# Kernel optimization log

Hardware: AMD Instinct MI355X
Metric: run time of the kernel (lower is better)

Reference implementation:

```python
import jax, jax.numpy as jnp
import numpy as np

N = 84          # nodes; N*(N-1)/2 == 3486, hardcoded by LayerNorm shapes
P = 3486        # number of pairwise rows
H = 2048        # h_size
EPS = 1e-5


def _gru_cell(x, h, Wih, Whh, bih, bhh):
    # PyTorch GRUCell math. Wih: [3H, in], Whh: [3H, H]
    gi = x @ Wih.T + bih
    gh = h @ Whh.T + bhh
    ir, iz, inew = jnp.split(gi, 3, axis=1)
    hr, hz, hnew = jnp.split(gh, 3, axis=1)
    r = jax.nn.sigmoid(ir + hr)
    z = jax.nn.sigmoid(iz + hz)
    n = jnp.tanh(inew + r * hnew)
    return (1.0 - z) * n + z * h


def _full_ln(x, w, b):
    # nn.LayerNorm([3486, h]) normalizes over BOTH dims jointly (biased var)
    mu = jnp.mean(x)
    var = jnp.mean((x - mu) ** 2)
    return (x - mu) * jax.lax.rsqrt(var + EPS) * w + b


def setup_inputs() -> dict:
    key = jax.random.key(0)
    ks = jax.random.split(key, 22)
    f32 = jnp.float32

    def nrm(k, shape, std):
        return jax.random.normal(k, shape, dtype=f32) * std

    h2 = H // 2
    return {
        "x": nrm(ks[0], (N, 64), 1.0),
        "hid": nrm(ks[1], (P, H), 1.0),
        # GRUCell(64, H) parameters
        "gru_Wih": nrm(ks[2], (3 * H, 64), 1.0 / np.sqrt(64)),
        "gru_Whh": nrm(ks[3], (3 * H, H), 1.0 / np.sqrt(H)),
        "gru_bih": nrm(ks[4], (3 * H,), 0.01),
        "gru_bhh": nrm(ks[5], (3 * H,), 0.01),
        # Linear/LayerNorm stack
        "W1": nrm(ks[6], (H, H), np.sqrt(2.0 / H)),
        "b1": jnp.zeros((H,), f32),
        "ln1_w": jnp.ones((P, H), f32),
        "ln1_b": jnp.zeros((P, H), f32),
        "W2": nrm(ks[7], (h2, H), np.sqrt(2.0 / H)),
        "b2": jnp.zeros((h2,), f32),
        "ln2_w": jnp.ones((P, h2), f32),
        "ln2_b": jnp.zeros((P, h2), f32),
        "W3": nrm(ks[8], (h2, h2), np.sqrt(2.0 / h2)),
        "b3": jnp.zeros((h2,), f32),
        "ln3_w": jnp.ones((P, h2), f32),
        "ln3_b": jnp.zeros((P, h2), f32),
        "W4": nrm(ks[9], (1, h2), np.sqrt(2.0 / h2)),
        "b4": jnp.zeros((1,), f32),
    }


def reference(x, hid, gru_Wih, gru_Whh, gru_bih, gru_bhh,
              W1, b1, ln1_w, ln1_b, W2, b2, ln2_w, ln2_b,
              W3, b3, ln3_w, ln3_b, W4, b4):
    # Pairwise gather: rows ordered (0,1),(0,2),...,(0,N-1),(1,2),... -- matches
    # the torch loop of expand+cat.
    iu, ju = jnp.triu_indices(N, k=1)
    x1 = x[iu]  # [P, 64]
    x2 = x[ju]  # [P, 64]

    h = _gru_cell(x1, hid, gru_Wih, gru_Whh, gru_bih, gru_bhh)
    h = _gru_cell(x2, h, gru_Wih, gru_Whh, gru_bih, gru_bhh)

    h = _full_ln(jax.nn.relu(h @ W1.T + b1), ln1_w, ln1_b)
    h = _full_ln(jax.nn.relu(h @ W2.T + b2), ln2_w, ln2_b)
    h = _full_ln(jax.nn.relu(h @ W3.T + b3), ln3_w, ln3_b)
    vals = jax.nn.sigmoid(h @ W4.T + b4)[:, 0]  # [P]

    # Strict-upper-triangular scatter + symmetrize (equals the torch pad loop)
    M = jnp.zeros((N, N), dtype=vals.dtype).at[iu, ju].set(vals)
    return M + M.T
```

## Files before the change

kernel.cpp:

```cpp
#include <hip/hip_runtime.h>
#include <stdint.h>

#define P_PAIRS 3486
#define NNODES 84
#define HSZ 2048
#define H2SZ 1024
#define G3H 6144
#define LN_EPS 1e-5f

typedef short bf16x8 __attribute__((ext_vector_type(8)));
typedef float f32x4 __attribute__((ext_vector_type(4)));

typedef __attribute__((address_space(3))) unsigned int lds_uint;
typedef __attribute__((address_space(1))) const unsigned int global_cuint;

__device__ __forceinline__ unsigned short f2bf(float f) {
    unsigned int u = __float_as_uint(f);
    return (unsigned short)((u + 0x7fffu + ((u >> 16) & 1u)) >> 16);
}
__device__ __forceinline__ float bf2f(unsigned short s) {
    return __uint_as_float(((unsigned int)s) << 16);
}
__device__ __forceinline__ float sigm(float x) {
    return 1.f / (1.f + expf(-x));
}

#define S_WHH (G3H * HSZ / 4)
#define S_W1  (HSZ * HSZ / 4)
#define S_W2  (H2SZ * HSZ / 4)
#define S_W3  (H2SZ * H2SZ / 4)
#define S_HID (P_PAIRS * HSZ / 4)
#define B0 (S_WHH)
#define B1 (B0 + S_W1)
#define B2 (B1 + S_W2)
#define B3 (B2 + S_W3)
#define B4 (B3 + S_HID)

__device__ __forceinline__ void cvt4(const float4* in, ushort4* out, int i) {
    float4 v = in[i];
    ushort4 o;
    o.x = f2bf(v.x); o.y = f2bf(v.y); o.z = f2bf(v.z); o.w = f2bf(v.w);
    out[i] = o;
}

__global__ void k_prep(const float4* __restrict__ Whh, ushort4* __restrict__ whh_b,
                       const float4* __restrict__ W1, ushort4* __restrict__ w1_b,
                       const float4* __restrict__ W2, ushort4* __restrict__ w2_b,
                       const float4* __restrict__ W3, ushort4* __restrict__ w3_b,
                       const float4* __restrict__ hid, ushort4* __restrict__ hid_b,
                       int* __restrict__ ip, int* __restrict__ jp, float* __restrict__ acc,
                       const float* __restrict__ x, const float* __restrict__ Wih,
                       const float* __restrict__ bih, float* __restrict__ gi) {
    const int tid0 = blockIdx.x * blockDim.x + threadIdx.x;
    const int stride = gridDim.x * blockDim.x;
    int idx = tid0;
    if (idx < 8) acc[idx] = 0.f;
    if (idx < P_PAIRS) {
        int i = 0, rem = idx;
        while (rem >= NNODES - 1 - i) { rem -= NNODES - 1 - i; ++i; }
        ip[idx] = i;
        jp[idx] = i + 1 + rem;
    }
    for (; idx < B4; idx += stride) {
        if (idx < B0)      cvt4(Whh, whh_b, idx);
        else if (idx < B1) cvt4(W1, w1_b, idx - B0);
        else if (idx < B2) cvt4(W2, w2_b, idx - B1);
        else if (idx < B3) cvt4(W3, w3_b, idx - B2);
        else               cvt4(hid, hid_b, idx - B3);
    }
    for (int g = tid0; g < NNODES * G3H; g += stride) {
        int node = g / G3H, n = g - node * G3H;
        const float* xr = x + node * 64;
        const float* wr = Wih + (size_t)n * 64;
        float s = bih[n];
#pragma unroll
        for (int k = 0; k < 64; ++k) s += xr[k] * wr[k];
        gi[g] = s;
    }
}

__global__ __launch_bounds__(256)
void k_gemm(const unsigned short* __restrict__ A, const unsigned short* __restrict__ B,
            const float* __restrict__ bias, float* __restrict__ Cf,
            unsigned short* __restrict__ Cb,
            int M, int N, int K, int relu, float* __restrict__ accg, int redslot) {
    __shared__ __align__(16) unsigned short lsA[128 * 32];
    __shared__ __align__(16) unsigned short lsB[128 * 32];
    const int m0 = blockIdx.x * 128;
    const int n0 = blockIdx.y * 128;
    const int tid = threadIdx.x;
    const int lane = tid & 63;
    const int wave = tid >> 6;
    const int wr = (wave >> 1) * 64;
    const int wc = (wave & 1) * 64;
    const int fr = lane & 15;
    const int quad = lane >> 4;
    const int kof = quad * 8;

    f32x4 acc[4][4];
#pragma unroll
    for (int i = 0; i < 4; ++i)
#pragma unroll
        for (int j = 0; j < 4; ++j) {
            f32x4 z = {0.f, 0.f, 0.f, 0.f};
            acc[i][j] = z;
        }

    const int lin0 = (wave * 2) * 1024 + lane * 16;
    const int lin1 = lin0 + 1024;
    const int row0 = lin0 >> 6, col0 = (lin0 & 63) >> 1;
    const int row1 = lin1 >> 6, col1 = (lin1 & 63) >> 1;
    int ga0 = m0 + row0; if (ga0 >= M) ga0 = M - 1;
    int ga1 = m0 + row1; if (ga1 >= M) ga1 = M - 1;
    const int gb0 = n0 + row0, gb1 = n0 + row1;

    const unsigned short* pa0 = A + (size_t)ga0 * K + col0;
    const unsigned short* pa1 = A + (size_t)ga1 * K + col1;
    const unsigned short* pb0 = B + (size_t)gb0 * K + col0;
    const unsigned short* pb1 = B + (size_t)gb1 * K + col1;
    lds_uint* la0 = (lds_uint*)&lsA[(wave * 2) * 512];
    lds_uint* la1 = (lds_uint*)&lsA[(wave * 2 + 1) * 512];
    lds_uint* lb0 = (lds_uint*)&lsB[(wave * 2) * 512];
    lds_uint* lb1 = (lds_uint*)&lsB[(wave * 2 + 1) * 512];

    for (int k0 = 0; k0 < K; k0 += 32) {
        __syncthreads();
        __builtin_amdgcn_global_load_lds((global_cuint*)(pa0 + k0), la0, 16, 0, 0);
        __builtin_amdgcn_global_load_lds((global_cuint*)(pa1 + k0), la1, 16, 0, 0);
        __builtin_amdgcn_global_load_lds((global_cuint*)(pb0 + k0), lb0, 16, 0, 0);
        __builtin_amdgcn_global_load_lds((global_cuint*)(pb1 + k0), lb1, 16, 0, 0);
        __syncthreads();
        bf16x8 av[4], bv[4];
#pragma unroll
        for (int mi = 0; mi < 4; ++mi)
            av[mi] = *(const bf16x8*)(&lsA[(wr + mi * 16 + fr) * 32 + kof]);
#pragma unroll
        for (int ni = 0; ni < 4; ++ni)
            bv[ni] = *(const bf16x8*)(&lsB[(wc + ni * 16 + fr) * 32 + kof]);
#pragma unroll
        for (int mi = 0; mi < 4; ++mi)
#pragma unroll
            for (int ni = 0; ni < 4; ++ni)
                acc[mi][ni] = __builtin_amdgcn_mfma_f32_16x16x32_bf16(av[mi], bv[ni], acc[mi][ni], 0, 0, 0);
    }

    float s1 = 0.f, s2 = 0.f;
#pragma unroll
    for (int mi = 0; mi < 4; ++mi) {
#pragma unroll
        for (int r = 0; r < 4; ++r) {
            int row = m0 + wr + mi * 16 + quad * 4 + r;
            if (row >= M) continue;
#pragma unroll
            for (int ni = 0; ni < 4; ++ni) {
                int col = n0 + wc + ni * 16 + fr;
                float v = acc[mi][ni][r];
                if (bias) v += bias[col];
                if (relu) v = fmaxf(v, 0.f);
                if (redslot >= 0) { s1 += v; s2 += v * v; }
                if (Cb) Cb[(size_t)row * N + col] = f2bf(v);
                else    Cf[(size_t)row * N + col] = v;
            }
        }
    }

    if (redslot >= 0) {
        __syncthreads();
        float* sm = (float*)lsA;
        sm[tid] = s1;
        sm[256 + tid] = s2;
        __syncthreads();
        for (int o = 128; o > 0; o >>= 1) {
            if (tid < o) {
                sm[tid] += sm[tid + o];
                sm[256 + tid] += sm[256 + tid + o];
            }
            __syncthreads();
        }
        if (tid == 0) {
            atomicAdd(&accg[redslot * 2], sm[0]);
            atomicAdd(&accg[redslot * 2 + 1], sm[256]);
        }
    }
}

__global__ void k_combine(const float4* __restrict__ gi, const ushort4* __restrict__ gh,
                          const int* __restrict__ pair, const float4* __restrict__ hprev_f,
                          const ushort4* __restrict__ hprev_b,
                          ushort4* __restrict__ hout) {
    int idx = blockIdx.x * blockDim.x + threadIdx.x;
    if (idx >= P_PAIRS * (HSZ / 4)) return;
    int p = idx >> 9;
    int c4 = idx & 511;
    int node = pair[p];
    const float4* gip = gi + (size_t)node * (G3H / 4) + c4;
    const ushort4* ghp = gh + (size_t)p * (G3H / 4) + c4;
    float4 gir = gip[0],   giz = gip[512], gin = gip[1024];
    ushort4 ghr4 = ghp[0], ghz4 = ghp[512], ghn4 = ghp[1024];
    float hr[4] = {bf2f(ghr4.x), bf2f(ghr4.y), bf2f(ghr4.z), bf2f(ghr4.w)};
    float hz[4] = {bf2f(ghz4.x), bf2f(ghz4.y), bf2f(ghz4.z), bf2f(ghz4.w)};
    float hn[4] = {bf2f(ghn4.x), bf2f(ghn4.y), bf2f(ghn4.z), bf2f(ghn4.w)};
    float hp[4];
    if (hprev_f) {
        float4 h = hprev_f[idx];
        hp[0] = h.x; hp[1] = h.y; hp[2] = h.z; hp[3] = h.w;
    } else {
        ushort4 h = hprev_b[idx];
        hp[0] = bf2f(h.x); hp[1] = bf2f(h.y); hp[2] = bf2f(h.z); hp[3] = bf2f(h.w);
    }
    float ir[4] = {gir.x, gir.y, gir.z, gir.w};
    float iz[4] = {giz.x, giz.y, giz.z, giz.w};
    float in_[4] = {gin.x, gin.y, gin.z, gin.w};
    unsigned short o[4];
#pragma unroll
    for (int q = 0; q < 4; ++q) {
        float r = sigm(ir[q] + hr[q]);
        float z = sigm(iz[q] + hz[q]);
        float nn = tanhf(in_[q] + r * hn[q]);
        o[q] = f2bf((1.f - z) * nn + z * hp[q]);
    }
    ushort4 ov = {o[0], o[1], o[2], o[3]};
    hout[idx] = ov;
}

__global__ void k_lnapply(const float4* __restrict__ t, const float4* __restrict__ w,
                          const float4* __restrict__ b, const float* __restrict__ acc, int slot,
                          int n, ushort4* __restrict__ out) {
    float cnt = (float)n;
    float mu = acc[slot * 2] / cnt;
    float var = acc[slot * 2 + 1] / cnt - mu * mu;
    float inv = rsqrtf(var + LN_EPS);
    int n4 = n >> 2;
    int idx = blockIdx.x * blockDim.x + threadIdx.x;
    int stride = gridDim.x * blockDim.x;
    for (; idx < n4; idx += stride) {
        float4 tv = t[idx], wv = w[idx], bv = b[idx];
        ushort4 o;
        o.x = f2bf((tv.x - mu) * inv * wv.x + bv.x);
        o.y = f2bf((tv.y - mu) * inv * wv.y + bv.y);
        o.z = f2bf((tv.z - mu) * inv * wv.z + bv.z);
        o.w = f2bf((tv.w - mu) * inv * wv.w + bv.w);
        out[idx] = o;
    }
}

__global__ void k_head(const float* __restrict__ t, const float* __restrict__ w,
                       const float* __restrict__ b, const float* __restrict__ accv,
                       const float* __restrict__ W4, const float* __restrict__ b4,
                       float* __restrict__ vals) {
    float cnt = (float)P_PAIRS * (float)H2SZ;
    float mu = accv[4] / cnt;
    float var = accv[5] / cnt - mu * mu;
    float inv = rsqrtf(var + LN_EPS);
    int wid = (blockIdx.x * blockDim.x + threadIdx.x) >> 6;
    int lane = threadIdx.x & 63;
    if (wid >= P_PAIRS) return;
    const float* row = t + (size_t)wid * H2SZ;
    const float* wrp = w + (size_t)wid * H2SZ;
    const float* brp = b + (size_t)wid * H2SZ;
    float s = 0.f;
    for (int k = lane; k < H2SZ; k += 64)
        s += ((row[k] - mu) * inv * wrp[k] + brp[k]) * W4[k];
#pragma unroll
    for (int o = 32; o > 0; o >>= 1) s += __shfl_down(s, o, 64);
    if (lane == 0) vals[wid] = sigm(s + b4[0]);
}

__global__ void k_out(const float* __restrict__ vals, float* __restrict__ out) {
    int idx = blockIdx.x * blockDim.x + threadIdx.x;
    if (idx >= NNODES * NNODES) return;
    int r = idx / NNODES, c = idx - r * NNODES;
    if (r == c) { out[idx] = 0.f; return; }
    int i = r < c ? r : c, j = r < c ? c : r;
    int p = i * (NNODES - 1) - i * (i - 1) / 2 + (j - i - 1);
    out[idx] = vals[p];
}

extern "C" void kernel_launch(void* const* d_in, const int* in_sizes, int n_in,
                              void* d_out, int out_size, void* d_ws, size_t ws_size,
                              hipStream_t stream) {
    const float* x    = (const float*)d_in[0];
    const float* hid  = (const float*)d_in[1];
    const float* Wih  = (const float*)d_in[2];
    const float* Whh  = (const float*)d_in[3];
    const float* bih  = (const float*)d_in[4];
    const float* bhh  = (const float*)d_in[5];
    const float* W1   = (const float*)d_in[6];
    const float* b1   = (const float*)d_in[7];
    const float* ln1w = (const float*)d_in[8];
    const float* ln1b = (const float*)d_in[9];
    const float* W2   = (const float*)d_in[10];
    const float* b2   = (const float*)d_in[11];
    const float* ln2w = (const float*)d_in[12];
    const float* ln2b = (const float*)d_in[13];
    const float* W3   = (const float*)d_in[14];
    const float* b3   = (const float*)d_in[15];
    const float* ln3w = (const float*)d_in[16];
    const float* ln3b = (const float*)d_in[17];
    const float* W4   = (const float*)d_in[18];
    const float* b4   = (const float*)d_in[19];
    float* out = (float*)d_out;

    char* ws = (char*)d_ws;
    size_t off = 0;
    auto alloc = [&](size_t bytes) -> void* {
        off = (off + 255) & ~(size_t)255;
        void* p = ws + off;
        off += bytes;
        return p;
    };

    float* acc            = (float*)alloc(8 * sizeof(float));
    int*   ip             = (int*)alloc(P_PAIRS * sizeof(int));
    int*   jp             = (int*)alloc(P_PAIRS * sizeof(int));
    float* gi             = (float*)alloc((size_t)NNODES * G3H * sizeof(float));
    unsigned short* whh_b = (unsigned short*)alloc((size_t)G3H * HSZ * 2);
    unsigned short* w1_b  = (unsigned short*)alloc((size_t)HSZ * HSZ * 2);
    unsigned short* w2_b  = (unsigned short*)alloc((size_t)H2SZ * HSZ * 2);
    unsigned short* w3_b  = (unsigned short*)alloc((size_t)H2SZ * H2SZ * 2);
    unsigned short* hid_b = (unsigned short*)alloc((size_t)P_PAIRS * HSZ * 2);
    unsigned short* hbuf  = (unsigned short*)alloc((size_t)P_PAIRS * HSZ * 2);
    unsigned short* gh    = (unsigned short*)alloc((size_t)P_PAIRS * G3H * 2);
    float* t              = (float*)alloc((size_t)P_PAIRS * HSZ * sizeof(float));
    float* vals           = (float*)alloc((size_t)P_PAIRS * sizeof(float));
    (void)ws_size; (void)in_sizes; (void)n_in; (void)out_size;

    unsigned short* lnb = hid_b;

    k_prep<<<2048, 256, 0, stream>>>((const float4*)Whh, (ushort4*)whh_b,
                                     (const float4*)W1, (ushort4*)w1_b,
                                     (const float4*)W2, (ushort4*)w2_b,
                                     (const float4*)W3, (ushort4*)w3_b,
                                     (const float4*)hid, (ushort4*)hid_b,
                                     ip, jp, acc, x, Wih, bih, gi);

    dim3 gBig((P_PAIRS + 127) / 128, G3H / 128);
    dim3 g3((P_PAIRS + 127) / 128, HSZ / 128);
    dim3 g4((P_PAIRS + 127) / 128, H2SZ / 128);
    int cgrid = (P_PAIRS * HSZ / 4 + 255) / 256;

    k_gemm<<<gBig, 256, 0, stream>>>(hid_b, whh_b, bhh, nullptr, gh, P_PAIRS, G3H, HSZ, 0, acc, -1);
    k_combine<<<cgrid, 256, 0, stream>>>((const float4*)gi, (const ushort4*)gh, ip,
                                         (const float4*)hid, nullptr, (ushort4*)hbuf);
    k_gemm<<<gBig, 256, 0, stream>>>(hbuf, whh_b, bhh, nullptr, gh, P_PAIRS, G3H, HSZ, 0, acc, -1);
    k_combine<<<cgrid, 256, 0, stream>>>((const float4*)gi, (const ushort4*)gh, jp,
                                         nullptr, (const ushort4*)hbuf, (ushort4*)hbuf);

    k_gemm<<<g3, 256, 0, stream>>>(hbuf, w1_b, b1, t, nullptr, P_PAIRS, HSZ, HSZ, 1, acc, 0);
    k_lnapply<<<2048, 256, 0, stream>>>((const float4*)t, (const float4*)ln1w, (const float4*)ln1b,
                                        acc, 0, P_PAIRS * HSZ, (ushort4*)lnb);

    k_gemm<<<g4, 256, 0, stream>>>(lnb, w2_b, b2, t, nullptr, P_PAIRS, H2SZ, HSZ, 1, acc, 1);
    k_lnapply<<<2048, 256, 0, stream>>>((const float4*)t, (const float4*)ln2w, (const float4*)ln2b,
                                        acc, 1, P_PAIRS * H2SZ, (ushort4*)lnb);

    k_gemm<<<g4, 256, 0, stream>>>(lnb, w3_b, b3, t, nullptr, P_PAIRS, H2SZ, H2SZ, 1, acc, 2);

    k_head<<<(P_PAIRS * 64 + 255) / 256, 256, 0, stream>>>(t, ln3w, ln3b, acc, W4, b4, vals);

    k_out<<<(NNODES * NNODES + 255) / 256, 256, 0, stream>>>(vals, out);
}
```

Measured before the change: 828.4 us.

## Double-buffer GEMM LDS tiles with two-deep async global-to-LDS prefetch

Splits the GEMM kernel's A/B shared-memory tiles into two buffers and prefetches the tile two K-steps ahead with global_load_lds. The MFMA work on one buffer can then overlap with loads into the other. Each iteration waits with explicit vmcnt counts and raw s_barrier instead of a load-then-sync sequence. This doubles LDS use per block, which may lower occupancy, and correctness now depends on the hand-set waitcnt encoding.

```diff
diff --git a/kernel.cpp b/kernel.cpp
--- a/kernel.cpp
+++ b/kernel.cpp
@@ -13,6 +13,8 @@
 
 typedef __attribute__((address_space(3))) unsigned int lds_uint;
 typedef __attribute__((address_space(1))) const unsigned int global_cuint;
+
+#define WAIT_VM(n) __builtin_amdgcn_s_waitcnt(0x0F00 | 0x70 | ((n) & 0xF) | (((n) >> 4) << 14))
 
 __device__ __forceinline__ unsigned short f2bf(float f) {
     unsigned int u = __float_as_uint(f);
@@ -84,8 +86,8 @@
             const float* __restrict__ bias, float* __restrict__ Cf,
             unsigned short* __restrict__ Cb,
             int M, int N, int K, int relu, float* __restrict__ accg, int redslot) {
-    __shared__ __align__(16) unsigned short lsA[128 * 32];
-    __shared__ __align__(16) unsigned short lsB[128 * 32];
+    __shared__ __align__(16) unsigned short lsA[2][128 * 32];
+    __shared__ __align__(16) unsigned short lsB[2][128 * 32];
     const int m0 = blockIdx.x * 128;
     const int n0 = blockIdx.y * 128;
     const int tid = threadIdx.x;
@@ -118,30 +120,45 @@
     const unsigned short* pa1 = A + (size_t)ga1 * K + col1;
     const unsigned short* pb0 = B + (size_t)gb0 * K + col0;
     const unsigned short* pb1 = B + (size_t)gb1 * K + col1;
-    lds_uint* la0 = (lds_uint*)&lsA[(wave * 2) * 512];
-    lds_uint* la1 = (lds_uint*)&lsA[(wave * 2 + 1) * 512];
-    lds_uint* lb0 = (lds_uint*)&lsB[(wave * 2) * 512];
-    lds_uint* lb1 = (lds_uint*)&lsB[(wave * 2 + 1) * 512];
-
-    for (int k0 = 0; k0 < K; k0 += 32) {
-        __syncthreads();
-        __builtin_amdgcn_global_load_lds((global_cuint*)(pa0 + k0), la0, 16, 0, 0);
-        __builtin_amdgcn_global_load_lds((global_cuint*)(pa1 + k0), la1, 16, 0, 0);
-        __builtin_amdgcn_global_load_lds((global_cuint*)(pb0 + k0), lb0, 16, 0, 0);
-        __builtin_amdgcn_global_load_lds((global_cuint*)(pb1 + k0), lb1, 16, 0, 0);
-        __syncthreads();
+    const int ch0 = (wave * 2) * 512;
+    const int ch1 = ch0 + 512;
+
+    auto dma_tile = [&](int k0, int b) {
+        __builtin_amdgcn_global_load_lds((global_cuint*)(pa0 + k0), (lds_uint*)&lsA[b][ch0], 16, 0, 0);
+        __builtin_amdgcn_global_load_lds((global_cuint*)(pa1 + k0), (lds_uint*)&lsA[b][ch1], 16, 0, 0);
+        __builtin_amdgcn_global_load_lds((global_cuint*)(pb0 + k0), (lds_uint*)&lsB[b][ch0], 16, 0, 0);
+        __builtin_amdgcn_global_load_lds((global_cuint*)(pb1 + k0), (lds_uint*)&lsB[b][ch1], 16, 0, 0);
+    };
+
+    dma_tile(0, 0);
+    dma_tile(32, 1);
+    WAIT_VM(4);
+    __builtin_amdgcn_s_barrier();
+
+    const int T = K >> 5;
+    for (int it = 0; it < T; ++it) {
+        const int cur = it & 1;
         bf16x8 av[4], bv[4];
 #pragma unroll
         for (int mi = 0; mi < 4; ++mi)
-            av[mi] = *(const bf16x8*)(&lsA[(wr + mi * 16 + fr) * 32 + kof]);
+            av[mi] = *(const bf16x8*)(&lsA[cur][(wr + mi * 16 + fr) * 32 + kof]);
 #pragma unroll
         for (int ni = 0; ni < 4; ++ni)
-            bv[ni] = *(const bf16x8*)(&lsB[(wc + ni * 16 + fr) * 32 + kof]);
+            bv[ni] = *(const bf16x8*)(&lsB[cur][(wc + ni * 16 + fr) * 32 + kof]);
 #pragma unroll
         for (int mi = 0; mi < 4; ++mi)
 #pragma unroll
             for (int ni = 0; ni < 4; ++ni)
                 acc[mi][ni] = __builtin_amdgcn_mfma_f32_16x16x32_bf16(av[mi], bv[ni], acc[mi][ni], 0, 0, 0);
+        __builtin_amdgcn_s_barrier();
+        const int kpre = (it + 2) << 5;
+        if (kpre < K) {
+            dma_tile(kpre, cur);
+            WAIT_VM(4);
+        } else if (it + 1 < T) {
+            WAIT_VM(0);
+        }
+        __builtin_amdgcn_s_barrier();
     }
 
     float s1 = 0.f, s2 = 0.f;
@@ -166,7 +183,7 @@
 
     if (redslot >= 0) {
         __syncthreads();
-        float* sm = (float*)lsA;
+        float* sm = (float*)&lsA[0][0];
         sm[tid] = s1;
         sm[256 + tid] = s2;
         __syncthreads();
```

Result: no change. 833.1 us (+0.6%).

## Store GEMM intermediates as bf16, fuse output scatter into head, add occupancy bound

Applied to the files above, without the earlier changes.

The linear-layer GEMM outputs are now written as bf16 instead of fp32, and the layernorm-apply and head kernels read bf16. This halves intermediate traffic. The first GRU combine reads the bf16 copy of hid instead of the fp32 input. The separate output kernel is removed, and the head kernel scatters each value symmetrically into the matrix and zeroes the diagonal. k_gemm also gets a min-blocks-per-CU launch bound. The cost is lower precision of pre-LN activations, and the launch bound may cause register spills; layernorm statistics are still accumulated in fp32 inside the GEMM.

```diff
diff --git a/kernel.cpp b/kernel.cpp
--- a/kernel.cpp
+++ b/kernel.cpp
@@ -79,7 +79,7 @@
     }
 }
 
-__global__ __launch_bounds__(256)
+__global__ __launch_bounds__(256, 4)
 void k_gemm(const unsigned short* __restrict__ A, const unsigned short* __restrict__ B,
             const float* __restrict__ bias, float* __restrict__ Cf,
             unsigned short* __restrict__ Cb,
@@ -185,8 +185,7 @@
 }
 
 __global__ void k_combine(const float4* __restrict__ gi, const ushort4* __restrict__ gh,
-                          const int* __restrict__ pair, const float4* __restrict__ hprev_f,
-                          const ushort4* __restrict__ hprev_b,
+                          const int* __restrict__ pair, const ushort4* __restrict__ hprev,
                           ushort4* __restrict__ hout) {
     int idx = blockIdx.x * blockDim.x + threadIdx.x;
     if (idx >= P_PAIRS * (HSZ / 4)) return;
@@ -200,14 +199,8 @@
     float hr[4] = {bf2f(ghr4.x), bf2f(ghr4.y), bf2f(ghr4.z), bf2f(ghr4.w)};
     float hz[4] = {bf2f(ghz4.x), bf2f(ghz4.y), bf2f(ghz4.z), bf2f(ghz4.w)};
     float hn[4] = {bf2f(ghn4.x), bf2f(ghn4.y), bf2f(ghn4.z), bf2f(ghn4.w)};
-    float hp[4];
-    if (hprev_f) {
-        float4 h = hprev_f[idx];
-        hp[0] = h.x; hp[1] = h.y; hp[2] = h.z; hp[3] = h.w;
-    } else {
-        ushort4 h = hprev_b[idx];
-        hp[0] = bf2f(h.x); hp[1] = bf2f(h.y); hp[2] = bf2f(h.z); hp[3] = bf2f(h.w);
-    }
+    ushort4 h = hprev[idx];
+    float hp[4] = {bf2f(h.x), bf2f(h.y), bf2f(h.z), bf2f(h.w)};
     float ir[4] = {gir.x, gir.y, gir.z, gir.w};
     float iz[4] = {giz.x, giz.y, giz.z, giz.w};
     float in_[4] = {gin.x, gin.y, gin.z, gin.w};
@@ -223,7 +216,7 @@
     hout[idx] = ov;
 }
 
-__global__ void k_lnapply(const float4* __restrict__ t, const float4* __restrict__ w,
+__global__ void k_lnapply(const ushort4* __restrict__ t, const float4* __restrict__ w,
                           const float4* __restrict__ b, const float* __restrict__ acc, int slot,
                           int n, ushort4* __restrict__ out) {
     float cnt = (float)n;
@@ -234,46 +227,44 @@
     int idx = blockIdx.x * blockDim.x + threadIdx.x;
     int stride = gridDim.x * blockDim.x;
     for (; idx < n4; idx += stride) {
-        float4 tv = t[idx], wv = w[idx], bv = b[idx];
+        ushort4 tv = t[idx];
+        float4 wv = w[idx], bv = b[idx];
         ushort4 o;
-        o.x = f2bf((tv.x - mu) * inv * wv.x + bv.x);
-        o.y = f2bf((tv.y - mu) * inv * wv.y + bv.y);
-        o.z = f2bf((tv.z - mu) * inv * wv.z + bv.z);
-        o.w = f2bf((tv.w - mu) * inv * wv.w + bv.w);
+        o.x = f2bf((bf2f(tv.x) - mu) * inv * wv.x + bv.x);
+        o.y = f2bf((bf2f(tv.y) - mu) * inv * wv.y + bv.y);
+        o.z = f2bf((bf2f(tv.z) - mu) * inv * wv.z + bv.z);
+        o.w = f2bf((bf2f(tv.w) - mu) * inv * wv.w + bv.w);
         out[idx] = o;
     }
 }
 
-__global__ void k_head(const float* __restrict__ t, const float* __restrict__ w,
+__global__ void k_head(const unsigned short* __restrict__ t, const float* __restrict__ w,
                        const float* __restrict__ b, const float* __restrict__ accv,
                        const float* __restrict__ W4, const float* __restrict__ b4,
-                       float* __restrict__ vals) {
+                       const int* __restrict__ ip, const int* __restrict__ jp,
+                       float* __restrict__ out) {
+    int wid = (blockIdx.x * blockDim.x + threadIdx.x) >> 6;
+    int lane = threadIdx.x & 63;
+    if (wid >= P_PAIRS) return;
+    if (lane == 0 && wid < NNODES) out[wid * NNODES + wid] = 0.f;
     float cnt = (float)P_PAIRS * (float)H2SZ;
     float mu = accv[4] / cnt;
     float var = accv[5] / cnt - mu * mu;
     float inv = rsqrtf(var + LN_EPS);
-    int wid = (blockIdx.x * blockDim.x + threadIdx.x) >> 6;
-    int lane = threadIdx.x & 63;
-    if (wid >= P_PAIRS) return;
-    const float* row = t + (size_t)wid * H2SZ;
+    const unsigned short* row = t + (size_t)wid * H2SZ;
     const float* wrp = w + (size_t)wid * H2SZ;
     const float* brp = b + (size_t)wid * H2SZ;
     float s = 0.f;
     for (int k = lane; k < H2SZ; k += 64)
-        s += ((row[k] - mu) * inv * wrp[k] + brp[k]) * W4[k];
+        s += ((bf2f(row[k]) - mu) * inv * wrp[k] + brp[k]) * W4[k];
 #pragma unroll
     for (int o = 32; o > 0; o >>= 1) s += __shfl_down(s, o, 64);
-    if (lane == 0) vals[wid] = sigm(s + b4[0]);
-}
-
-__global__ void k_out(const float* __restrict__ vals, float* __restrict__ out) {
-    int idx = blockIdx.x * blockDim.x + threadIdx.x;
-    if (idx >= NNODES * NNODES) return;
-    int r = idx / NNODES, c = idx - r * NNODES;
-    if (r == c) { out[idx] = 0.f; return; }
-    int i = r < c ? r : c, j = r < c ? c : r;
-    int p = i * (NNODES - 1) - i * (i - 1) / 2 + (j - i - 1);
-    out[idx] = vals[p];
+    if (lane == 0) {
+        float v = sigm(s + b4[0]);
+        int i = ip[wid], j = jp[wid];
+        out[i * NNODES + j] = v;
+        out[j * NNODES + i] = v;
+    }
 }
 
 extern "C" void kernel_launch(void* const* d_in, const int* in_sizes, int n_in,
@@ -321,8 +312,7 @@
     unsigned short* hid_b = (unsigned short*)alloc((size_t)P_PAIRS * HSZ * 2);
     unsigned short* hbuf  = (unsigned short*)alloc((size_t)P_PAIRS * HSZ * 2);
     unsigned short* gh    = (unsigned short*)alloc((size_t)P_PAIRS * G3H * 2);
-    float* t              = (float*)alloc((size_t)P_PAIRS * HSZ * sizeof(float));
-    float* vals           = (float*)alloc((size_t)P_PAIRS * sizeof(float));
+    unsigned short* t_b   = (unsigned short*)alloc((size_t)P_PAIRS * HSZ * 2);
     (void)ws_size; (void)in_sizes; (void)n_in; (void)out_size;
 
     unsigned short* lnb = hid_b;
@@ -341,22 +331,20 @@
 
     k_gemm<<<gBig, 256, 0, stream>>>(hid_b, whh_b, bhh, nullptr, gh, P_PAIRS, G3H, HSZ, 0, acc, -1);
     k_combine<<<cgrid, 256, 0, stream>>>((const float4*)gi, (const ushort4*)gh, ip,
-                                         (const float4*)hid, nullptr, (ushort4*)hbuf);
+                                         (const ushort4*)hid_b, (ushort4*)hbuf);
     k_gemm<<<gBig, 256, 0, stream>>>(hbuf, whh_b, bhh, nullptr, gh, P_PAIRS, G3H, HSZ, 0, acc, -1);
     k_combine<<<cgrid, 256, 0, stream>>>((const float4*)gi, (const ushort4*)gh, jp,
-                                         nullptr, (const ushort4*)hbuf, (ushort4*)hbuf);
-
-    k_gemm<<<g3, 256, 0, stream>>>(hbuf, w1_b, b1, t, nullptr, P_PAIRS, HSZ, HSZ, 1, acc, 0);
-    k_lnapply<<<2048, 256, 0, stream>>>((const float4*)t, (const float4*)ln1w, (const float4*)ln1b,
+                                         (const ushort4*)hbuf, (ushort4*)hbuf);
+
+    k_gemm<<<g3, 256, 0, stream>>>(hbuf, w1_b, b1, nullptr, t_b, P_PAIRS, HSZ, HSZ, 1, acc, 0);
+    k_lnapply<<<2048, 256, 0, stream>>>((const ushort4*)t_b, (const float4*)ln1w, (const float4*)ln1b,
                                         acc, 0, P_PAIRS * HSZ, (ushort4*)lnb);
 
-    k_gemm<<<g4, 256, 0, stream>>>(lnb, w2_b, b2, t, nullptr, P_PAIRS, H2SZ, HSZ, 1, acc, 1);
-    k_lnapply<<<2048, 256, 0, stream>>>((const float4*)t, (const float4*)ln2w, (const float4*)ln2b,
+    k_gemm<<<g4, 256, 0, stream>>>(lnb, w2_b, b2, nullptr, t_b, P_PAIRS, H2SZ, HSZ, 1, acc, 1);
+    k_lnapply<<<2048, 256, 0, stream>>>((const ushort4*)t_b, (const float4*)ln2w, (const float4*)ln2b,
                                         acc, 1, P_PAIRS * H2SZ, (ushort4*)lnb);
 
-    k_gemm<<<g4, 256, 0, stream>>>(lnb, w3_b, b3, t, nullptr, P_PAIRS, H2SZ, H2SZ, 1, acc, 2);
-
-    k_head<<<(P_PAIRS * 64 + 255) / 256, 256, 0, stream>>>(t, ln3w, ln3b, acc, W4, b4, vals);
-
-    k_out<<<(NNODES * NNODES + 255) / 256, 256, 0, stream>>>(vals, out);
-}
+    k_gemm<<<g4, 256, 0, stream>>>(lnb, w3_b, b3, nullptr, t_b, P_PAIRS, H2SZ, H2SZ, 1, acc, 2);
+
+    k_head<<<(P_PAIRS * 64 + 255) / 256, 256, 0, stream>>>(t_b, ln3w, ln3b, acc, W4, b4, ip, jp, out);
+}
```

New measurement: 745.7 us. 10.0% less time.
